# Kernel optimization log

Measured on AMD Instinct MI355X. Metric: run time of the kernel, lower is better.

## Reference

```python
import jax, jax.numpy as jnp
import numpy as np

B, NEG = 2, 16            # queries, negatives per query
N, E, D = 10000, 80000, 128  # nodes, edges, feature dim (in_dim == out_dim)
NUM_REL = 237
L = 3                     # PNA layers
NODE_RATIO = 0.1
K = max(1, int(NODE_RATIO * N))  # static top-k: every repeated graph has exactly N nodes
EPS = 1e-5


def _score(hidden, rel, lin_W, lin_b, m1_W, m1_b, m2_W, m2_b):
    heur = jnp.concatenate([hidden, rel], axis=-1) @ lin_W + lin_b
    x = heur * hidden
    h = jax.nn.relu(x @ m1_W + m1_b)
    return jnp.squeeze(h @ m2_W + m2_b, -1)


def _pna_conv(hidden, src, dst, emask, deg, pre_W, pre_b, post_W, post_b, out_W, out_b):
    """PNA layer with mean/max/min/std aggregators and identity/amplification/attenuation
    scalers, restricted to edges where emask is True. deg is the (clamped >=1) degree used
    by the scalers."""
    BN = hidden.shape[0]
    # message: pre-linear on [x_i (target), x_j (source)] per edge  -> (Erep, D)
    m = jnp.concatenate([hidden[dst], hidden[src]], axis=-1) @ pre_W + pre_b
    w = emask.astype(hidden.dtype)[:, None]
    cnt = jax.ops.segment_sum(emask.astype(hidden.dtype), dst, num_segments=BN)
    denom = jnp.maximum(cnt, 1.0)[:, None]
    s1 = jax.ops.segment_sum(m * w, dst, num_segments=BN)
    s2 = jax.ops.segment_sum(m * m * w, dst, num_segments=BN)
    mean = s1 / denom
    var = jax.nn.relu(s2 / denom - mean * mean)
    std = jnp.sqrt(var + EPS)
    has = (cnt > 0)[:, None]
    mx = jnp.where(has, jax.ops.segment_max(jnp.where(emask[:, None], m, -jnp.inf), dst, num_segments=BN), 0.0)
    mn = jnp.where(has, jax.ops.segment_min(jnp.where(emask[:, None], m, jnp.inf), dst, num_segments=BN), 0.0)
    agg = jnp.concatenate([mean, mx, mn, std], axis=-1)           # (BN, 4D)
    logd = jnp.log(deg + 1.0)                                     # deg >= 1 -> logd > 0
    avg_log = jnp.mean(logd)
    agg = jnp.concatenate([agg, agg * (logd / avg_log)[:, None], agg * (avg_log / logd)[:, None]], axis=-1)  # (BN, 12D)
    return (agg @ post_W + post_b) @ out_W + out_b


def _forward(h_index, r_index, t_index, hidden_states, edge_index, rel_embedding,
             lin_W, lin_b, m1_W, m1_b, m2_W, m2_b, pre_W, pre_b, post_W, post_b, out_W, out_b):
    sc = (lin_W, lin_b, m1_W, m1_b, m2_W, m2_b)
    # negative_sample_to_tail
    is_t_neg = jnp.all(h_index == h_index[:, :1], axis=-1, keepdims=True)
    h_idx = jnp.where(is_t_neg, h_index, t_index)
    t_idx = jnp.where(is_t_neg, t_index, h_index)
    r_idx = jnp.where(is_t_neg, r_index, r_index + NUM_REL)
    # repeat_graph
    offsets = jnp.arange(B, dtype=h_idx.dtype) * N               # (B,)
    src = jnp.tile(edge_index[0], B) + jnp.repeat(offsets, E)    # (B*E,)
    dst = jnp.tile(edge_index[1], B) + jnp.repeat(offsets, E)
    BN = B * N
    rel_embeds = rel_embedding[r_idx[:, 0]].astype(hidden_states.dtype)  # (B, D)
    flat_h = h_idx[:, 0] + offsets
    flat_t = t_idx[:, 0] + offsets
    # literal `repeat_interleave(N, dim=0)[:B]` quirk -> row arange(B)//N of gathered embs
    sel = jnp.arange(B) // N
    h_vals = hidden_states[h_idx[:, 0]][sel]                     # (B, D)
    t_vals = hidden_states[t_idx[:, 0]][sel]
    # init_input_embeds: boundary condition + initial score at head nodes
    boundary = jnp.zeros((BN, D), hidden_states.dtype).at[flat_t].set(t_vals).at[flat_h].set(h_vals)
    score = jnp.zeros(BN, jnp.float32).at[flat_h].set(_score(h_vals, rel_embeds, *sc))
    hidden = boundary
    rel_per_node = jnp.repeat(rel_embeds, N, axis=0)             # (BN, D), rel_embeds[batch_rep]
    rows = jnp.arange(B)[:, None]
    for l in range(L):
        # select_edges_pyg with degree_ratio=1.0: all out-edges of per-graph top-k nodes
        _, idx = jax.lax.top_k(score.reshape(B, N), K)           # (B, K)
        node_sel = jnp.zeros((B, N), bool).at[rows, idx].set(True).reshape(-1)
        emask = node_sel[src]                                    # (B*E,) selected-edge mask
        out_deg = jax.ops.segment_sum(emask.astype(jnp.float32), src, num_segments=BN)
        deg_sub = jnp.maximum(out_deg.astype(hidden.dtype), 1.0)
        new_hidden = _pna_conv(hidden, src, dst, emask, deg_sub,
                               pre_W[l], pre_b[l], post_W[l], post_b[l], out_W[l], out_b[l])
        # residual only for nodes with selected outgoing edges
        hidden = jnp.where((out_deg > 0)[:, None], hidden + new_hidden, hidden)
        score = _score(hidden, rel_per_node, *sc)
    # read out scores at (repeated) tail indices -> (B, NEG)
    return score[t_idx + offsets[:, None]]


def setup_inputs() -> dict:
    key = jax.random.key(0)
    ks = jax.random.split(key, 14)
    s = 0.05
    hi = jax.random.randint(ks[0], (B, 1), 0, N)
    h_index = jnp.tile(hi, (1, NEG))                 # constant per row (assert in forward)
    r0 = jax.random.randint(ks[1], (B, 1), 0, NUM_REL)
    r_index = jnp.tile(r0, (1, NEG))                 # constant per row (assert in forward)
    t_index = jax.random.randint(ks[2], (B, NEG), 0, N)
    hidden_states = jax.random.normal(ks[3], (N, D), jnp.float32)
    edge_index = jax.random.randint(ks[4], (2, E), 0, N)
    return {
        "h_index": h_index, "r_index": r_index, "t_index": t_index,
        "hidden_states": hidden_states, "edge_index": edge_index,
        "rel_embedding": jax.random.normal(ks[5], (2 * NUM_REL, D), jnp.float32) * s,
        "lin_W": jax.random.normal(ks[6], (2 * D, D), jnp.float32) * s, "lin_b": jnp.zeros(D, jnp.float32),
        "m1_W": jax.random.normal(ks[7], (D, D), jnp.float32) * s, "m1_b": jnp.zeros(D, jnp.float32),
        "m2_W": jax.random.normal(ks[8], (D, 1), jnp.float32) * s, "m2_b": jnp.zeros(1, jnp.float32),
        "pre_W": jax.random.normal(ks[9], (L, 2 * D, D), jnp.float32) * s, "pre_b": jnp.zeros((L, D), jnp.float32),
        "post_W": jax.random.normal(ks[10], (L, 12 * D, D), jnp.float32) * s, "post_b": jnp.zeros((L, D), jnp.float32),
        "out_W": jax.random.normal(ks[11], (L, D, D), jnp.float32) * s, "out_b": jnp.zeros((L, D), jnp.float32),
    }


def reference(h_index, r_index, t_index, hidden_states, edge_index, rel_embedding,
              lin_W, lin_b, m1_W, m1_b, m2_W, m2_b, pre_W, pre_b, post_W, post_b, out_W, out_b):
    return _forward(h_index, r_index, t_index, hidden_states, edge_index, rel_embedding,
                    lin_W, lin_b, m1_W, m1_b, m2_W, m2_b, pre_W, pre_b, post_W, post_b, out_W, out_b)
```

## Files before the change

kernel.cpp:

```cpp
#include <hip/hip_runtime.h>
#include <math.h>

#define Bq 2
#define NEG 16
#define Nn 10000
#define Ee 80000
#define Dd 128
#define NUM_REL 237
#define Ll 3
#define K_SEL 1000
#define BN (Bq*Nn)
#define EPSV 1e-5f
#define MAXACT 2048
#define MAXTOUCH 8192
#define SELCAP 3328
#define LN2F 0.69314718056f

constexpr size_t HID_OFF   = 0;
constexpr size_t SCORE_OFF = HID_OFF   + (size_t)BN*Dd*4;
constexpr size_t CVEC_OFF  = SCORE_OFF + (size_t)BN*4;
constexpr size_t HDR_OFF   = CVEC_OFF  + (size_t)Bq*Dd*4;
constexpr size_t THR_OFF   = HDR_OFF   + 64*4;
constexpr size_t SEL_OFF   = THR_OFF   + Bq*8;
constexpr size_t DEG_OFF   = SEL_OFF   + (size_t)BN*4;
constexpr size_t SLOT_OFF  = DEG_OFF   + (size_t)BN*4;
constexpr size_t CNT_OFF   = SLOT_OFF  + (size_t)BN*4;
constexpr size_t SDEG_OFF  = CNT_OFF   + (size_t)MAXACT*4;
constexpr size_t S1_OFF    = SDEG_OFF  + (size_t)MAXACT*4;
constexpr size_t S2_OFF    = S1_OFF    + (size_t)MAXACT*Dd*4;
constexpr size_t MXB_OFF   = S2_OFF    + (size_t)MAXACT*Dd*4;
constexpr size_t MNB_OFF   = MXB_OFF   + (size_t)MAXACT*Dd*4;
constexpr size_t TPART_OFF = MNB_OFF   + (size_t)MAXACT*Dd*4;
constexpr size_t ALIST_OFF = TPART_OFF + (size_t)4*MAXACT*Dd*4;
constexpr size_t FLAG_OFF  = ALIST_OFF + (size_t)MAXACT*4;
constexpr size_t TLIST_OFF = FLAG_OFF  + (size_t)BN*4;
constexpr size_t EDGE_OFF  = TLIST_OFF + (size_t)MAXTOUCH*4;
constexpr size_t CTR_OFF   = EDGE_OFF  + (size_t)Bq*Ee*2*4;

__device__ __forceinline__ unsigned encf(float f){
  unsigned u = __float_as_uint(f);
  return (u & 0x80000000u) ? ~u : (u | 0x80000000u);
}
__device__ __forceinline__ float decf(unsigned e){
  unsigned u = (e & 0x80000000u) ? (e & 0x7FFFFFFFu) : ~e;
  return __uint_as_float(u);
}
__device__ __forceinline__ unsigned long long make_key(float f, int i){
  unsigned d = ~encf(f);
  return ((unsigned long long)d << 32) | (unsigned)i;
}

__global__ void k_zero(float* hidden, unsigned* flag){
  int i = blockIdx.x*blockDim.x + threadIdx.x;
  if (i < BN*Dd/4) ((float4*)hidden)[i] = make_float4(0.f,0.f,0.f,0.f);
  if (i < BN) flag[i] = 0u;
}

__global__ __launch_bounds__(256) void k_prep(
    const int* h_index, const int* r_index, const int* t_index,
    const float* hidden_states, const float* rel_embedding,
    const float* lin_W, const float* lin_b, const float* m1_W, const float* m1_b,
    const float* m2_W, const float* m2_b,
    int* hdr, float* cvec, float* hidden, float* score,
    unsigned* flag, int* tlist, unsigned* ctr){
  __shared__ int sh_fh[Bq], sh_ft[Bq], sh_r0[Bq], sh_hsrc, sh_tsrc;
  __shared__ float s_relv[Bq][Dd], s_cvec[Bq][Dd], s_hv[Dd], s_x[Bq][Dd], s_p[Bq][Dd];
  __shared__ float s_s0[Dd];
  __shared__ float sc0_sh;
  int tid = threadIdx.x;
  if (tid == 0){
    int n = 0;
    for (int b=0;b<Bq;b++){
      bool eq = true;
      for (int j=1;j<NEG;j++) eq = eq && (h_index[b*NEG+j]==h_index[b*NEG]);
      int h0 = eq ? h_index[b*NEG] : t_index[b*NEG];
      int t0 = eq ? t_index[b*NEG] : h_index[b*NEG];
      int r0 = eq ? r_index[b*NEG] : r_index[b*NEG] + NUM_REL;
      sh_fh[b] = h0 + b*Nn; sh_ft[b] = t0 + b*Nn; sh_r0[b] = r0;
      hdr[0+b] = sh_fh[b]; hdr[2+b] = sh_ft[b];
      for (int j=0;j<NEG;j++){
        int tj = eq ? t_index[b*NEG+j] : h_index[b*NEG+j];
        hdr[4 + b*NEG + j] = tj + b*Nn;
      }
      if (b==0){ sh_hsrc = h0; sh_tsrc = t0; }
      if (!flag[sh_ft[b]]){ flag[sh_ft[b]] = 1u; tlist[n++] = sh_ft[b]; }
      if (!flag[sh_fh[b]]){ flag[sh_fh[b]] = 1u; tlist[n++] = sh_fh[b]; }
    }
    ctr[3] = (unsigned)n;
  }
  __syncthreads();
  int b = tid >> 7, d = tid & 127;
  s_relv[b][d] = rel_embedding[(size_t)sh_r0[b]*Dd + d];
  if (b == 0){
    s_hv[d] = hidden_states[(size_t)sh_hsrc*Dd + d];
    s_s0[d] = fmaxf(m1_b[d], 0.f) * m2_W[d];
  }
  __syncthreads();
  if (tid == 0){
    float s = m2_b[0];
    for (int k=0;k<Dd;k++) s += s_s0[k];
    sc0_sh = s;
    ctr[4] = __float_as_uint(s);
  }
  float acc = lin_b[d];
  for (int k=0;k<Dd;k++) acc += s_relv[b][k]*lin_W[(Dd+k)*Dd + d];
  s_cvec[b][d] = acc; cvec[b*Dd+d] = acc;
  hidden[(size_t)sh_ft[b]*Dd + d] = hidden_states[(size_t)sh_tsrc*Dd + d];
  hidden[(size_t)sh_fh[b]*Dd + d] = hidden_states[(size_t)sh_hsrc*Dd + d];
  __syncthreads();
  float sc0 = sc0_sh;
  for (int i = tid; i < BN; i += 256) score[i] = sc0;
  float hv = s_hv[d];
  float heur = s_cvec[b][d];
  for (int k=0;k<Dd;k++) heur += s_hv[k]*lin_W[k*Dd + d];
  s_x[b][d] = heur * hv;
  __syncthreads();
  float a2 = m1_b[d];
  for (int k=0;k<Dd;k++) a2 += s_x[b][k]*m1_W[k*Dd + d];
  s_p[b][d] = fmaxf(a2, 0.f) * m2_W[d];
  __syncthreads();
  if (tid < Bq){
    float s = m2_b[0];
    for (int k=0;k<Dd;k++) s += s_p[tid][k];
    score[sh_fh[tid]] = s;
  }
}

__global__ __launch_bounds__(256) void k_select(
    const float* score, const int* tlist, const unsigned* ctr,
    unsigned long long* thr){
  int b = blockIdx.x;
  int nt = (int)ctr[3];
  unsigned d0 = ~encf(__uint_as_float(ctr[4]));
  __shared__ unsigned sd[SELCAP];
  __shared__ unsigned short sidx[SELCAP];
  __shared__ unsigned hist[256], histT[256];
  __shared__ int ntb_sh;
  __shared__ unsigned long long pref_sh;
  __shared__ unsigned kk_sh;
  int tid = threadIdx.x;
  if (tid==0){ ntb_sh = 0; pref_sh = 0ull; kk_sh = K_SEL; }
  __syncthreads();
  int vlo = b*Nn, vhi = vlo + Nn;
  for (int i = tid; i < nt; i += 256){
    int v = tlist[i];
    if (v >= vlo && v < vhi){
      int pos = atomicAdd(&ntb_sh, 1);
      if (pos < SELCAP){
        sd[pos] = ~encf(score[v]);
        sidx[pos] = (unsigned short)(v - vlo);
      }
    }
  }
  __syncthreads();
  int ntb = min(ntb_sh, SELCAP);
  unsigned nvirt = (unsigned)(Nn - ntb);
  for (int pass = 7; pass >= 0; --pass){
    hist[tid] = 0u; histT[tid] = 0u;
    __syncthreads();
    unsigned long long pref = pref_sh;
    int sh_hi = 8*(pass+1);
    for (int j = tid; j < ntb; j += 256){
      unsigned long long key = ((unsigned long long)sd[j] << 32) | (unsigned long long)sidx[j];
      bool ok = (pass==7) || ((key >> sh_hi) == (pref >> sh_hi));
      if (ok) atomicAdd(&hist[(unsigned)(key >> (8*pass)) & 255u], 1u);
      if (pass < 4){
        unsigned idx = sidx[j];
        bool oki = (pass == 3) || ((idx >> sh_hi) == (((unsigned)pref) >> sh_hi));
        if (oki) atomicAdd(&histT[(idx >> (8*pass)) & 255u], 1u);
      }
    }
    __syncthreads();
    if (pass >= 4){
      if (tid == 0){
        unsigned long long keyv_hi = ((unsigned long long)d0 << 32);
        bool ok = (pass==7) || ((keyv_hi >> sh_hi) == (pref >> sh_hi));
        if (ok) atomicAdd(&hist[(d0 >> (8*(pass-4))) & 255u], nvirt);
      }
    } else {
      if ((unsigned)(pref >> 32) == d0){
        unsigned long long hf = 0ull;
        if (pass < 3) hf = (unsigned long long)((((unsigned)pref) >> sh_hi)) << sh_hi;
        unsigned long long lo = hf + ((unsigned long long)tid << (8*pass));
        unsigned long long hi = lo + (1ull << (8*pass));
        unsigned long long nn = (unsigned long long)Nn;
        unsigned long long l2 = lo < nn ? lo : nn;
        unsigned long long h2 = hi < nn ? hi : nn;
        if (h2 > l2){
          unsigned c = (unsigned)(h2 - l2) - histT[tid];
          if (c > 0u) atomicAdd(&hist[tid], c);
        }
      }
    }
    __syncthreads();
    if (tid < 256){
      unsigned kk = kk_sh;
      unsigned cum = 0;
      for (int i=0;i<tid;i++) cum += hist[i];
      unsigned h = hist[tid];
      if (h > 0u && cum < kk && kk <= cum + h){
        pref_sh |= ((unsigned long long)tid) << (8*pass);
        kk_sh = kk - cum;
      }
    }
    __syncthreads();
  }
  if (tid==0) thr[b] = pref_sh;
}

__global__ void k_mask(const float* score, const unsigned long long* thr, unsigned* sel,
                       unsigned* out_deg, float* s1, float* s2,
                       unsigned* mxb, unsigned* mnb, unsigned* cnt, unsigned* ctr){
  int i = blockIdx.x*blockDim.x + threadIdx.x;
  if (i < BN){
    int b = i / Nn; int v = i - b*Nn;
    sel[i] = (make_key(score[i], v) <= thr[b]) ? 1u : 0u;
    out_deg[i] = 0u;
  }
  if (i < MAXACT*Dd){ s1[i]=0.f; s2[i]=0.f; mxb[i]=0u; mnb[i]=0xFFFFFFFFu; }
  if (i < MAXACT) cnt[i]=0u;
  if (i < 3) ctr[i]=0u;
}

__global__ void k_degree(const int* ei, const unsigned* sel, unsigned* out_deg){
  int e = blockIdx.x*blockDim.x + threadIdx.x;
  if (e >= Ee) return;
  int s0 = ei[e];
  #pragma unroll
  for (int b=0;b<Bq;b++){
    int v = s0 + b*Nn;
    if (sel[v]) atomicAdd(&out_deg[v], 1u);
  }
}

__global__ void k_active(const unsigned* out_deg, int* node_slot, int* alist,
                         float* slot_deg, unsigned* ctr, unsigned* flag, int* tlist){
  int v = blockIdx.x*blockDim.x + threadIdx.x;
  if (v >= BN) return;
  unsigned dg = out_deg[v];
  if (dg > 0u){
    int slot = (int)atomicAdd(&ctr[0], 1u);
    alist[slot] = v; node_slot[v] = slot; slot_deg[slot] = (float)dg;
    atomicAdd((float*)&ctr[2], logf((float)dg + 1.0f));
    if (atomicExch(&flag[v], 1u) == 0u){
      int p = (int)atomicAdd(&ctr[3], 1u);
      tlist[p] = v;
    }
  }
}

__global__ void k_edges(const int* ei, const unsigned* sel, const unsigned* out_deg,
                        const int* node_slot, int* edges, unsigned* cnt, unsigned* ctr){
  int e = blockIdx.x*blockDim.x + threadIdx.x;
  if (e >= Ee) return;
  int s0 = ei[e], d0 = ei[Ee + e];
  #pragma unroll
  for (int b=0;b<Bq;b++){
    int s = s0 + b*Nn, dv = d0 + b*Nn;
    if (sel[s] && out_deg[dv] > 0u){
      int slot = node_slot[dv];
      int j = (int)atomicAdd(&ctr[1], 1u);
      edges[2*j] = s; edges[2*j+1] = slot;
      atomicAdd(&cnt[slot], 1u);
    }
  }
}

__global__ __launch_bounds__(128) void k_messages(
    const float* hidden, const int* edges, const int* alist,
    const float* preW, const float* preb,
    float* s1, float* s2, unsigned* mxb, unsigned* mnb, const unsigned* ctr){
  int ne = (int)ctr[1];
  int tid = threadIdx.x;
  __shared__ float sd[4][Dd], ss[4][Dd];
  __shared__ int dsl[4];
  float pb = preb[tid];
  for (int j0 = blockIdx.x*4; j0 < ne; j0 += gridDim.x*4){
    int nv = ne - j0; if (nv > 4) nv = 4;
    if (tid < 4){
      int j = j0 + ((tid < nv) ? tid : 0);
      dsl[tid] = edges[2*j+1];
    }
    #pragma unroll
    for (int e=0;e<4;e++){
      int j = j0 + ((e < nv) ? e : 0);
      int s = edges[2*j];
      int dv = alist[edges[2*j+1]];
      sd[e][tid] = hidden[(size_t)dv*Dd + tid];
      ss[e][tid] = hidden[(size_t)s*Dd + tid];
    }
    __syncthreads();
    float a[4] = {pb, pb, pb, pb};
    for (int k=0;k<Dd;k++){
      float w0 = preW[k*Dd + tid];
      float w1 = preW[(Dd+k)*Dd + tid];
      #pragma unroll
      for (int e=0;e<4;e++) a[e] += sd[e][k]*w0 + ss[e][k]*w1;
    }
    for (int e=0;e<nv;e++){
      int dslot = dsl[e];
      atomicAdd(&s1[dslot*Dd + tid], a[e]);
      atomicAdd(&s2[dslot*Dd + tid], a[e]*a[e]);
      atomicMax(&mxb[dslot*Dd + tid], encf(a[e]));
      atomicMin(&mnb[dslot*Dd + tid], encf(a[e]));
    }
    __syncthreads();
  }
}

__global__ __launch_bounds__(256) void k_post(
    const unsigned* cnt, const float* s1, const float* s2,
    const unsigned* mxb, const unsigned* mnb, const float* slot_deg,
    const float* postW, float* tpart, const unsigned* ctr){
  int na = (int)ctr[0];
  int bid = blockIdx.x;
  int tile = bid & 63, ch = (bid >> 6) & 3, half = bid >> 8;
  if (tile*32 >= na) return;
  float logsum = __uint_as_float(ctr[2]);
  float avg = (logsum + (float)(BN - na)*LN2F) / (float)BN;
  __shared__ float lb[32*Dd];
  __shared__ float sden[32];
  __shared__ unsigned shas[32];
  int tid = threadIdx.x;
  if (tid < 32){
    unsigned c = cnt[tile*32 + tid];
    sden[tid] = fmaxf((float)c, 1.0f);
    shas[tid] = c;
  }
  __syncthreads();
  for (int idx = tid; idx < 32*Dd; idx += 256){
    int sl = idx >> 7, kk = idx & 127;
    int gi = (tile*32 + sl)*Dd + kk;
    float den = sden[sl];
    float val;
    if (ch == 0)      val = s1[gi]/den;
    else if (ch == 1) val = shas[sl] ? decf(mxb[gi]) : 0.f;
    else if (ch == 2) val = shas[sl] ? decf(mnb[gi]) : 0.f;
    else {
      float mv = s1[gi]/den;
      float var = s2[gi]/den - mv*mv;
      val = sqrtf(fmaxf(var, 0.f) + EPSV);
    }
    lb[idx] = val;
  }
  __syncthreads();
  int cg = tid & 15, rg = tid >> 4;
  int ccol0 = half*64 + cg*4;
  float a0[2][4], a1[2][4], a2[2][4];
  #pragma unroll
  for (int i=0;i<2;i++)
    #pragma unroll
    for (int j=0;j<4;j++){ a0[i][j]=0.f; a1[i][j]=0.f; a2[i][j]=0.f; }
  for (int k4=0; k4<32; ++k4){
    float4 av[2];
    #pragma unroll
    for (int i=0;i<2;i++) av[i] = ((float4*)lb)[(rg*2+i)*32 + k4];
    #pragma unroll
    for (int j=0;j<4;j++){
      int krow = ch*128 + k4*4 + j;
      const float* wp = postW + (size_t)krow*Dd + ccol0;
      float4 w0 = *(const float4*)(wp);
      float4 w1 = *(const float4*)(wp + 512*Dd);
      float4 w2 = *(const float4*)(wp + 1024*Dd);
      #pragma unroll
      for (int i=0;i<2;i++){
        float a = (&av[i].x)[j];
        a0[i][0] += a*w0.x; a0[i][1] += a*w0.y; a0[i][2] += a*w0.z; a0[i][3] += a*w0.w;
        a1[i][0] += a*w1.x; a1[i][1] += a*w1.y; a1[i][2] += a*w1.z; a1[i][3] += a*w1.w;
        a2[i][0] += a*w2.x; a2[i][1] += a*w2.y; a2[i][2] += a*w2.z; a2[i][3] += a*w2.w;
      }
    }
  }
  #pragma unroll
  for (int i=0;i<2;i++){
    int slot = tile*32 + rg*2 + i;
    if (slot < na){
      float dg = slot_deg[slot];
      float logd = logf(dg + 1.f);
      float al = logd/avg, be = avg/logd;
      float4 r;
      r.x = a0[i][0] + al*a1[i][0] + be*a2[i][0];
      r.y = a0[i][1] + al*a1[i][1] + be*a2[i][1];
      r.z = a0[i][2] + al*a1[i][2] + be*a2[i][2];
      r.w = a0[i][3] + al*a1[i][3] + be*a2[i][3];
      *(float4*)(tpart + (size_t)ch*MAXACT*Dd + (size_t)slot*Dd + ccol0) = r;
    }
  }
}

__global__ __launch_bounds__(128) void k_out_resid(
    const float* tpart, const int* alist, const float* outW, const float* outb,
    const float* postb, float* hidden, const unsigned* ctr){
  int slot = blockIdx.x;
  if (slot >= (int)ctr[0]) return;
  int tid = threadIdx.x;
  __shared__ float tr[Dd];
  size_t o = (size_t)slot*Dd + tid;
  tr[tid] = tpart[o] + tpart[(size_t)MAXACT*Dd + o] + tpart[(size_t)2*MAXACT*Dd + o]
          + tpart[(size_t)3*MAXACT*Dd + o] + postb[tid];
  __syncthreads();
  int v = alist[slot];
  float acc = outb[tid];
  for (int k4=0;k4<32;k4++){
    float4 t4 = *(float4*)&tr[k4*4];
    acc += t4.x*outW[(k4*4+0)*Dd + tid];
    acc += t4.y*outW[(k4*4+1)*Dd + tid];
    acc += t4.z*outW[(k4*4+2)*Dd + tid];
    acc += t4.w*outW[(k4*4+3)*Dd + tid];
  }
  hidden[(size_t)v*Dd + tid] += acc;
}

__global__ __launch_bounds__(256) void k_score(
    const float* hidden, const float* cvec, const float* linW,
    const float* m1W, const float* m1b, const float* m2W, const float* m2b,
    const int* tlist, const unsigned* ctr, float* score){
  int nt = (int)ctr[3];
  int nb = blockIdx.x * 32;
  if (nb >= nt) return;
  __shared__ float sh[32*Dd];
  __shared__ float sx[32*Dd];
  __shared__ float sc[2*Dd];
  __shared__ int   sv[32];
  __shared__ float red[32*33];
  int tid = threadIdx.x;
  if (tid < 32){
    int idx = nb + tid;
    sv[tid] = (idx < nt) ? tlist[idx] : tlist[nb];
  }
  sc[tid] = cvec[tid];
  __syncthreads();
  for (int q = tid; q < 32*32; q += 256){
    int row = q >> 5, f4 = q & 31;
    ((float4*)sh)[row*32 + f4] = ((const float4*)(hidden + (size_t)sv[row]*Dd))[f4];
  }
  __syncthreads();
  int cg = tid & 31, rg = tid >> 5;
  int c0 = cg*4;
  float acc[4][4];
  #pragma unroll
  for (int i=0;i<4;i++){ acc[i][0]=0.f; acc[i][1]=0.f; acc[i][2]=0.f; acc[i][3]=0.f; }
  for (int k4=0;k4<32;k4++){
    float4 av[4];
    #pragma unroll
    for (int i=0;i<4;i++) av[i] = ((float4*)sh)[(rg*4+i)*32 + k4];
    #pragma unroll
    for (int j=0;j<4;j++){
      float4 w = *(const float4*)(linW + (size_t)(k4*4+j)*Dd + c0);
      #pragma unroll
      for (int i=0;i<4;i++){
        float a = (&av[i].x)[j];
        acc[i][0] += a*w.x; acc[i][1] += a*w.y; acc[i][2] += a*w.z; acc[i][3] += a*w.w;
      }
    }
  }
  #pragma unroll
  for (int i=0;i<4;i++){
    int row = rg*4 + i;
    int bb = (sv[row] >= Nn) ? 1 : 0;
    float4 cv = *(float4*)&sc[bb*Dd + c0];
    float4 hv = ((float4*)sh)[row*32 + cg];
    float4 x;
    x.x = (acc[i][0] + cv.x)*hv.x;
    x.y = (acc[i][1] + cv.y)*hv.y;
    x.z = (acc[i][2] + cv.z)*hv.z;
    x.w = (acc[i][3] + cv.w)*hv.w;
    ((float4*)sx)[row*32 + cg] = x;
  }
  __syncthreads();
  #pragma unroll
  for (int i=0;i<4;i++){ acc[i][0]=0.f; acc[i][1]=0.f; acc[i][2]=0.f; acc[i][3]=0.f; }
  for (int k4=0;k4<32;k4++){
    float4 av[4];
    #pragma unroll
    for (int i=0;i<4;i++) av[i] = ((float4*)sx)[(rg*4+i)*32 + k4];
    #pragma unroll
    for (int j=0;j<4;j++){
      float4 w = *(const float4*)(m1W + (size_t)(k4*4+j)*Dd + c0);
      #pragma unroll
      for (int i=0;i<4;i++){
        float a = (&av[i].x)[j];
        acc[i][0] += a*w.x; acc[i][1] += a*w.y; acc[i][2] += a*w.z; acc[i][3] += a*w.w;
      }
    }
  }
  float4 mb = *(const float4*)(m1b + c0);
  float4 mw = *(const float4*)(m2W + c0);
  #pragma unroll
  for (int i=0;i<4;i++){
    float p0 = fmaxf(acc[i][0]+mb.x, 0.f)*mw.x;
    float p1 = fmaxf(acc[i][1]+mb.y, 0.f)*mw.y;
    float p2 = fmaxf(acc[i][2]+mb.z, 0.f)*mw.z;
    float p3 = fmaxf(acc[i][3]+mb.w, 0.f)*mw.w;
    red[(rg*4+i)*33 + cg] = p0+p1+p2+p3;
  }
  __syncthreads();
  if (tid < 32){
    float s = m2b[0];
    for (int g=0; g<32; g++) s += red[tid*33 + g];
    if (nb + tid < nt) score[sv[tid]] = s;
  }
}

__global__ void k_gather(const float* score, const int* hdr, float* out){
  int i = threadIdx.x;
  if (i < Bq*NEG) out[i] = score[hdr[4+i]];
}

extern "C" void kernel_launch(void* const* d_in, const int* in_sizes, int n_in,
                              void* d_out, int out_size, void* d_ws, size_t ws_size,
                              hipStream_t stream){
  const int*   h_index       = (const int*)d_in[0];
  const int*   r_index       = (const int*)d_in[1];
  const int*   t_index       = (const int*)d_in[2];
  const float* hidden_states = (const float*)d_in[3];
  const int*   edge_index    = (const int*)d_in[4];
  const float* rel_embedding = (const float*)d_in[5];
  const float* lin_W  = (const float*)d_in[6];
  const float* lin_b  = (const float*)d_in[7];
  const float* m1_W   = (const float*)d_in[8];
  const float* m1_b   = (const float*)d_in[9];
  const float* m2_W   = (const float*)d_in[10];
  const float* m2_b   = (const float*)d_in[11];
  const float* pre_W  = (const float*)d_in[12];
  const float* pre_b  = (const float*)d_in[13];
  const float* post_W = (const float*)d_in[14];
  const float* post_b = (const float*)d_in[15];
  const float* out_W  = (const float*)d_in[16];
  const float* out_b  = (const float*)d_in[17];

  char* ws = (char*)d_ws;
  float*    hidden   = (float*)(ws + HID_OFF);
  float*    score    = (float*)(ws + SCORE_OFF);
  float*    cvec     = (float*)(ws + CVEC_OFF);
  int*      hdr      = (int*)(ws + HDR_OFF);
  unsigned long long* thr = (unsigned long long*)(ws + THR_OFF);
  unsigned* sel      = (unsigned*)(ws + SEL_OFF);
  unsigned* out_deg  = (unsigned*)(ws + DEG_OFF);
  int*      node_slot= (int*)(ws + SLOT_OFF);
  unsigned* cnt      = (unsigned*)(ws + CNT_OFF);
  float*    slot_deg = (float*)(ws + SDEG_OFF);
  float*    s1       = (float*)(ws + S1_OFF);
  float*    s2       = (float*)(ws + S2_OFF);
  unsigned* mxb      = (unsigned*)(ws + MXB_OFF);
  unsigned* mnb      = (unsigned*)(ws + MNB_OFF);
  float*    tpart    = (float*)(ws + TPART_OFF);
  int*      alist    = (int*)(ws + ALIST_OFF);
  unsigned* flag     = (unsigned*)(ws + FLAG_OFF);
  int*      tlist    = (int*)(ws + TLIST_OFF);
  int*      edges    = (int*)(ws + EDGE_OFF);
  unsigned* ctr      = (unsigned*)(ws + CTR_OFF);

  k_zero<<<(BN*Dd/4 + 255)/256, 256, 0, stream>>>(hidden, flag);
  k_prep<<<1, 256, 0, stream>>>(h_index, r_index, t_index, hidden_states, rel_embedding,
                                lin_W, lin_b, m1_W, m1_b, m2_W, m2_b,
                                hdr, cvec, hidden, score, flag, tlist, ctr);
  for (int l = 0; l < Ll; ++l){
    const float* preWl  = pre_W  + (size_t)l*2*Dd*Dd;
    const float* prebl  = pre_b  + (size_t)l*Dd;
    const float* postWl = post_W + (size_t)l*12*Dd*Dd;
    const float* postbl = post_b + (size_t)l*Dd;
    const float* outWl  = out_W  + (size_t)l*Dd*Dd;
    const float* outbl  = out_b  + (size_t)l*Dd;

    k_select<<<Bq, 256, 0, stream>>>(score, tlist, ctr, thr);
    k_mask<<<(MAXACT*Dd + 255)/256, 256, 0, stream>>>(score, thr, sel, out_deg,
                                                      s1, s2, mxb, mnb, cnt, ctr);
    k_degree<<<(Ee + 255)/256, 256, 0, stream>>>(edge_index, sel, out_deg);
    k_active<<<(BN + 255)/256, 256, 0, stream>>>(out_deg, node_slot, alist, slot_deg,
                                                 ctr, flag, tlist);
    k_edges<<<(Ee + 255)/256, 256, 0, stream>>>(edge_index, sel, out_deg, node_slot,
                                                edges, cnt, ctr);
    k_messages<<<512, 128, 0, stream>>>(hidden, edges, alist, preWl, prebl,
                                        s1, s2, mxb, mnb, ctr);
    k_post<<<512, 256, 0, stream>>>(cnt, s1, s2, mxb, mnb, slot_deg, postWl, tpart, ctr);
    k_out_resid<<<MAXACT, 128, 0, stream>>>(tpart, alist, outWl, outbl, postbl, hidden, ctr);
    k_score<<<MAXTOUCH/32, 256, 0, stream>>>(hidden, cvec, lin_W, m1_W, m1_b, m2_W, m2_b,
                                             tlist, ctr, score);
  }
  k_gather<<<1, 64, 0, stream>>>(score, hdr, (float*)d_out);
}
```

Before: 514.4 us.

## Tile post and out GEMMs through shared memory and trim last-layer scoring

k_post now uses 512-thread blocks covering the full output width and stages post_W rows through shared memory in 16-row chunks, with a padded activation buffer. k_out_resid processes 32 slots per block as a small tiled GEMM with out_W staged in shared memory instead of one slot per block. On the final layer k_score scores only the 32 query/negative nodes taken from the header list rather than every touched node. Unroll pragmas are added to several inner loops. Together these aim to cut redundant global weight reads and wasted scoring work, at the cost of more barriers and larger shared-memory use per block.

```diff
diff --git a/kernel.cpp b/kernel.cpp
--- a/kernel.cpp
+++ b/kernel.cpp
@@ -103,6 +103,7 @@
     ctr[4] = __float_as_uint(s);
   }
   float acc = lin_b[d];
+  #pragma unroll 8
   for (int k=0;k<Dd;k++) acc += s_relv[b][k]*lin_W[(Dd+k)*Dd + d];
   s_cvec[b][d] = acc; cvec[b*Dd+d] = acc;
   hidden[(size_t)sh_ft[b]*Dd + d] = hidden_states[(size_t)sh_tsrc*Dd + d];
@@ -112,10 +113,12 @@
   for (int i = tid; i < BN; i += 256) score[i] = sc0;
   float hv = s_hv[d];
   float heur = s_cvec[b][d];
+  #pragma unroll 8
   for (int k=0;k<Dd;k++) heur += s_hv[k]*lin_W[k*Dd + d];
   s_x[b][d] = heur * hv;
   __syncthreads();
   float a2 = m1_b[d];
+  #pragma unroll 8
   for (int k=0;k<Dd;k++) a2 += s_x[b][k]*m1_W[k*Dd + d];
   s_p[b][d] = fmaxf(a2, 0.f) * m2_W[d];
   __syncthreads();
@@ -291,6 +294,7 @@
     }
     __syncthreads();
     float a[4] = {pb, pb, pb, pb};
+    #pragma unroll 4
     for (int k=0;k<Dd;k++){
       float w0 = preW[k*Dd + tid];
       float w1 = preW[(Dd+k)*Dd + tid];
@@ -308,17 +312,18 @@
   }
 }
 
-__global__ __launch_bounds__(256) void k_post(
+__global__ __launch_bounds__(512) void k_post(
     const unsigned* cnt, const float* s1, const float* s2,
     const unsigned* mxb, const unsigned* mnb, const float* slot_deg,
     const float* postW, float* tpart, const unsigned* ctr){
   int na = (int)ctr[0];
   int bid = blockIdx.x;
-  int tile = bid & 63, ch = (bid >> 6) & 3, half = bid >> 8;
+  int tile = bid & 63, ch = bid >> 6;
   if (tile*32 >= na) return;
   float logsum = __uint_as_float(ctr[2]);
   float avg = (logsum + (float)(BN - na)*LN2F) / (float)BN;
-  __shared__ float lb[32*Dd];
+  __shared__ float lb[32*136];
+  __shared__ float wbuf[3*16*128];
   __shared__ float sden[32];
   __shared__ unsigned shas[32];
   int tid = threadIdx.x;
@@ -328,7 +333,7 @@
     shas[tid] = c;
   }
   __syncthreads();
-  for (int idx = tid; idx < 32*Dd; idx += 256){
+  for (int idx = tid; idx < 32*Dd; idx += 512){
     int sl = idx >> 7, kk = idx & 127;
     int gi = (tile*32 + sl)*Dd + kk;
     float den = sden[sl];
@@ -341,35 +346,46 @@
       float var = s2[gi]/den - mv*mv;
       val = sqrtf(fmaxf(var, 0.f) + EPSV);
     }
-    lb[idx] = val;
-  }
-  __syncthreads();
-  int cg = tid & 15, rg = tid >> 4;
-  int ccol0 = half*64 + cg*4;
+    lb[sl*136 + kk] = val;
+  }
+  int cg = tid & 31, rg = tid >> 5;
+  int c0 = cg*4;
   float a0[2][4], a1[2][4], a2[2][4];
   #pragma unroll
   for (int i=0;i<2;i++)
     #pragma unroll
     for (int j=0;j<4;j++){ a0[i][j]=0.f; a1[i][j]=0.f; a2[i][j]=0.f; }
-  for (int k4=0; k4<32; ++k4){
-    float4 av[2];
-    #pragma unroll
-    for (int i=0;i<2;i++) av[i] = ((float4*)lb)[(rg*2+i)*32 + k4];
-    #pragma unroll
-    for (int j=0;j<4;j++){
-      int krow = ch*128 + k4*4 + j;
-      const float* wp = postW + (size_t)krow*Dd + ccol0;
-      float4 w0 = *(const float4*)(wp);
-      float4 w1 = *(const float4*)(wp + 512*Dd);
-      float4 w2 = *(const float4*)(wp + 1024*Dd);
+  for (int chunk = 0; chunk < 8; ++chunk){
+    #pragma unroll
+    for (int i = 0; i < 3; ++i){
+      int f = tid + i*512;
+      int q = f >> 9, r = f & 511;
+      int kk = r >> 5, c4 = r & 31;
+      int grow = q*512 + ch*128 + chunk*16 + kk;
+      ((float4*)wbuf)[f] = *(const float4*)(postW + (size_t)grow*Dd + c4*4);
+    }
+    __syncthreads();
+    #pragma unroll
+    for (int k4 = 0; k4 < 4; ++k4){
+      float4 av0 = *(const float4*)&lb[(rg*2+0)*136 + chunk*16 + k4*4];
+      float4 av1 = *(const float4*)&lb[(rg*2+1)*136 + chunk*16 + k4*4];
       #pragma unroll
-      for (int i=0;i<2;i++){
-        float a = (&av[i].x)[j];
-        a0[i][0] += a*w0.x; a0[i][1] += a*w0.y; a0[i][2] += a*w0.z; a0[i][3] += a*w0.w;
-        a1[i][0] += a*w1.x; a1[i][1] += a*w1.y; a1[i][2] += a*w1.z; a1[i][3] += a*w1.w;
-        a2[i][0] += a*w2.x; a2[i][1] += a*w2.y; a2[i][2] += a*w2.z; a2[i][3] += a*w2.w;
-      }
-    }
+      for (int j = 0; j < 4; ++j){
+        int kk = k4*4 + j;
+        float4 w0 = *(const float4*)&wbuf[kk*128 + c0];
+        float4 w1 = *(const float4*)&wbuf[(16+kk)*128 + c0];
+        float4 w2 = *(const float4*)&wbuf[(32+kk)*128 + c0];
+        float av[2] = { (&av0.x)[j], (&av1.x)[j] };
+        #pragma unroll
+        for (int i=0;i<2;i++){
+          float a = av[i];
+          a0[i][0] += a*w0.x; a0[i][1] += a*w0.y; a0[i][2] += a*w0.z; a0[i][3] += a*w0.w;
+          a1[i][0] += a*w1.x; a1[i][1] += a*w1.y; a1[i][2] += a*w1.z; a1[i][3] += a*w1.w;
+          a2[i][0] += a*w2.x; a2[i][1] += a*w2.y; a2[i][2] += a*w2.z; a2[i][3] += a*w2.w;
+        }
+      }
+    }
+    __syncthreads();
   }
   #pragma unroll
   for (int i=0;i<2;i++){
@@ -383,39 +399,79 @@
       r.y = a0[i][1] + al*a1[i][1] + be*a2[i][1];
       r.z = a0[i][2] + al*a1[i][2] + be*a2[i][2];
       r.w = a0[i][3] + al*a1[i][3] + be*a2[i][3];
-      *(float4*)(tpart + (size_t)ch*MAXACT*Dd + (size_t)slot*Dd + ccol0) = r;
-    }
-  }
-}
-
-__global__ __launch_bounds__(128) void k_out_resid(
+      *(float4*)(tpart + (size_t)ch*MAXACT*Dd + (size_t)slot*Dd + c0) = r;
+    }
+  }
+}
+
+__global__ __launch_bounds__(256) void k_out_resid(
     const float* tpart, const int* alist, const float* outW, const float* outb,
     const float* postb, float* hidden, const unsigned* ctr){
-  int slot = blockIdx.x;
-  if (slot >= (int)ctr[0]) return;
+  int na = (int)ctr[0];
+  int tile = blockIdx.x;
+  if (tile*32 >= na) return;
+  __shared__ float tr[32*136];
+  __shared__ float wbuf[16*128];
   int tid = threadIdx.x;
-  __shared__ float tr[Dd];
-  size_t o = (size_t)slot*Dd + tid;
-  tr[tid] = tpart[o] + tpart[(size_t)MAXACT*Dd + o] + tpart[(size_t)2*MAXACT*Dd + o]
-          + tpart[(size_t)3*MAXACT*Dd + o] + postb[tid];
-  __syncthreads();
-  int v = alist[slot];
-  float acc = outb[tid];
-  for (int k4=0;k4<32;k4++){
-    float4 t4 = *(float4*)&tr[k4*4];
-    acc += t4.x*outW[(k4*4+0)*Dd + tid];
-    acc += t4.y*outW[(k4*4+1)*Dd + tid];
-    acc += t4.z*outW[(k4*4+2)*Dd + tid];
-    acc += t4.w*outW[(k4*4+3)*Dd + tid];
-  }
-  hidden[(size_t)v*Dd + tid] += acc;
+  for (int idx = tid; idx < 32*Dd; idx += 256){
+    int sl = idx >> 7, kk = idx & 127;
+    size_t o = (size_t)(tile*32 + sl)*Dd + kk;
+    tr[sl*136 + kk] = tpart[o] + tpart[(size_t)MAXACT*Dd + o]
+                    + tpart[(size_t)2*MAXACT*Dd + o] + tpart[(size_t)3*MAXACT*Dd + o]
+                    + postb[kk];
+  }
+  int cg = tid & 31, rg = tid >> 5;
+  int c0 = cg*4;
+  float4 ob = *(const float4*)(outb + c0);
+  float acc[4][4];
+  #pragma unroll
+  for (int r=0;r<4;r++){ acc[r][0]=ob.x; acc[r][1]=ob.y; acc[r][2]=ob.z; acc[r][3]=ob.w; }
+  for (int chunk = 0; chunk < 8; ++chunk){
+    #pragma unroll
+    for (int i = 0; i < 2; ++i){
+      int f = tid + i*256;
+      int kk = f >> 5, c4 = f & 31;
+      ((float4*)wbuf)[f] = *(const float4*)(outW + (size_t)(chunk*16 + kk)*Dd + c4*4);
+    }
+    __syncthreads();
+    #pragma unroll
+    for (int k4 = 0; k4 < 4; ++k4){
+      float4 av[4];
+      #pragma unroll
+      for (int r=0;r<4;r++)
+        av[r] = *(const float4*)&tr[(rg*4+r)*136 + chunk*16 + k4*4];
+      #pragma unroll
+      for (int j = 0; j < 4; ++j){
+        float4 w = *(const float4*)&wbuf[(k4*4+j)*128 + c0];
+        #pragma unroll
+        for (int r=0;r<4;r++){
+          float a = (&av[r].x)[j];
+          acc[r][0] += a*w.x; acc[r][1] += a*w.y; acc[r][2] += a*w.z; acc[r][3] += a*w.w;
+        }
+      }
+    }
+    __syncthreads();
+  }
+  #pragma unroll
+  for (int r=0;r<4;r++){
+    int slot = tile*32 + rg*4 + r;
+    if (slot < na){
+      int v = alist[slot];
+      float* hp = hidden + (size_t)v*Dd + c0;
+      float4 h4 = *(float4*)hp;
+      h4.x += acc[r][0]; h4.y += acc[r][1]; h4.z += acc[r][2]; h4.w += acc[r][3];
+      *(float4*)hp = h4;
+    }
+  }
 }
 
 __global__ __launch_bounds__(256) void k_score(
     const float* hidden, const float* cvec, const float* linW,
     const float* m1W, const float* m1b, const float* m2W, const float* m2b,
-    const int* tlist, const unsigned* ctr, float* score){
-  int nt = (int)ctr[3];
+    const int* tlist, const unsigned* ctr, float* score,
+    const int* ovr, int ovr_n){
+  int nt = (ovr_n > 0) ? ovr_n : (int)ctr[3];
+  const int* list = (ovr_n > 0) ? ovr : tlist;
   int nb = blockIdx.x * 32;
   if (nb >= nt) return;
   __shared__ float sh[32*Dd];
@@ -426,7 +482,7 @@
   int tid = threadIdx.x;
   if (tid < 32){
     int idx = nb + tid;
-    sv[tid] = (idx < nt) ? tlist[idx] : tlist[nb];
+    sv[tid] = (idx < nt) ? list[idx] : list[nb];
   }
   sc[tid] = cvec[tid];
   __syncthreads();
@@ -573,10 +629,16 @@
                                                 edges, cnt, ctr);
     k_messages<<<512, 128, 0, stream>>>(hidden, edges, alist, preWl, prebl,
                                         s1, s2, mxb, mnb, ctr);
-    k_post<<<512, 256, 0, stream>>>(cnt, s1, s2, mxb, mnb, slot_deg, postWl, tpart, ctr);
-    k_out_resid<<<MAXACT, 128, 0, stream>>>(tpart, alist, outWl, outbl, postbl, hidden, ctr);
-    k_score<<<MAXTOUCH/32, 256, 0, stream>>>(hidden, cvec, lin_W, m1_W, m1_b, m2_W, m2_b,
-                                             tlist, ctr, score);
+    k_post<<<256, 512, 0, stream>>>(cnt, s1, s2, mxb, mnb, slot_deg, postWl, tpart, ctr);
+    k_out_resid<<<MAXACT/32, 256, 0, stream>>>(tpart, alist, outWl, outbl, postbl,
+                                               hidden, ctr);
+    if (l < Ll-1){
+      k_score<<<MAXTOUCH/32, 256, 0, stream>>>(hidden, cvec, lin_W, m1_W, m1_b, m2_W, m2_b,
+                                               tlist, ctr, score, tlist, 0);
+    } else {
+      k_score<<<1, 256, 0, stream>>>(hidden, cvec, lin_W, m1_W, m1_b, m2_W, m2_b,
+                                     tlist, ctr, score, hdr + 4, Bq*NEG);
+    }
   }
   k_gather<<<1, 64, 0, stream>>>(score, hdr, (float*)d_out);
 }
```

After: 481.7 us. 1.07x faster.
